# Kernel optimization log

Measured on AMD Instinct MI355X. Metric: run time of the kernel, lower is better.

The kernel has to match this reference:

```python
import jax, jax.numpy as jnp
import numpy as np
from jax import lax

XI = 2.0
RADIUS = int(3 * XI)  # 6 -> kernel size 13


def _gaussian_weight(xi: float):
    radius = int(3 * xi)
    coords = jnp.arange(-radius, radius + 1, dtype=jnp.float32)
    g1 = jnp.exp(-coords ** 2 / (2.0 * xi * xi))
    g1 = g1 / g1.sum()
    g3 = g1[:, None, None] * g1[None, :, None] * g1[None, None, :]  # (K,K,K)
    # grouped conv weight: (out_ch=3, in_ch/groups=1, K, K, K), same kernel per channel
    return jnp.broadcast_to(g3[None, None], (3, 1) + g3.shape)


def setup_inputs() -> dict:
    key = jax.random.key(0)
    x = jax.random.normal(key, (1, 3, 192, 192, 192), dtype=jnp.float32)
    w = _gaussian_weight(XI)
    return {"x": x, "w": w}


def reference(x, w):
    # depthwise (groups=3) 3D cross-correlation with 'same' padding = radius,
    # matching nn.Conv3d(3, 3, (K,K,K), padding=radius, groups=3, bias=False)
    r = (w.shape[-1] - 1) // 2
    return lax.conv_general_dilated(
        x, w,
        window_strides=(1, 1, 1),
        padding=[(r, r)] * 3,
        dimension_numbers=("NCDHW", "OIDHW", "NCDHW"),
        feature_group_count=3,
    )
```

## Files before the change

kernel.cpp:

```cpp
#include <hip/hip_runtime.h>

#define RAD 6
#define KS 13
#define DIM 192
#define CH 3
#define W4C 48
#define PLANE4 (DIM * W4C)
#define VOL4 (DIM * PLANE4)
#define VOL (DIM * DIM * DIM)
#define TOTAL (CH * VOL)

__global__ void g1_extract_kernel(const float* __restrict__ w, float* __restrict__ g1) {
    int i = threadIdx.x;
    if (i < KS) {
        float s = 0.f;
        for (int j = 0; j < KS * KS; ++j) s += w[i * KS * KS + j];
        g1[i] = s;
    }
}

#define HT 32
#define HL 48
#define NT1 192
#define NLD (HL * W4C)

__global__ __launch_bounds__(NT1) void conv_wh2(const float* __restrict__ in,
                                                float* __restrict__ out,
                                                const float* __restrict__ g1) {
    __shared__ float4 tile[NLD];
    const int bid = blockIdx.x;
    const int ht = bid % 6;
    const int d = (bid / 6) % DIM;
    const int c = bid / (6 * DIM);
    const int h0 = ht * HT;
    const int t = threadIdx.x;

    float g[KS];
#pragma unroll
    for (int k = 0; k < KS; ++k) g[k] = g1[k];

    const float4* in4 = (const float4*)in;
    float4* out4 = (float4*)out;
    const size_t plane = (size_t)c * VOL4 + (size_t)d * PLANE4;
    const float4 z4 = make_float4(0.f, 0.f, 0.f, 0.f);

#pragma unroll
    for (int i = 0; i < 12; ++i) {
        int idx = t + i * NT1;
        int row = idx / W4C, w4 = idx % W4C;
        int h = h0 - 8 + row;
        int hc = min(max(h, 0), DIM - 1);
        float4 v = in4[plane + (size_t)hc * W4C + w4];
        if (h < 0 || h >= DIM) v = z4;
        tile[idx] = v;
    }
    __syncthreads();

    float4 va[12];
#pragma unroll
    for (int i = 0; i < 12; ++i) {
        int idx = t + i * NT1;
        int row = idx / W4C, w4 = idx % W4C;
        int w0 = w4 * 4;
        float f[20];
#pragma unroll
        for (int b = 0; b < 5; ++b) {
            int j = min(max(w4 + b - 2, 0), W4C - 1);
            float4 v = tile[row * W4C + j];
            f[4 * b + 0] = v.x; f[4 * b + 1] = v.y;
            f[4 * b + 2] = v.z; f[4 * b + 3] = v.w;
        }
#pragma unroll
        for (int j = 0; j < 20; ++j) {
            int ww = w0 - 8 + j;
            if (ww < 0 || ww >= DIM) f[j] = 0.f;
        }
        float4 o = z4;
#pragma unroll
        for (int k = 0; k < KS; ++k) {
            o.x += g[k] * f[k + 2];
            o.y += g[k] * f[k + 3];
            o.z += g[k] * f[k + 4];
            o.w += g[k] * f[k + 5];
        }
        va[i] = o;
    }
    __syncthreads();
#pragma unroll
    for (int i = 0; i < 12; ++i) tile[t + i * NT1] = va[i];
    __syncthreads();

    const int w4 = t % W4C;
    const int rg = t / W4C;
    const int i0 = rg * 8;
    float4 buf[KS];
#pragma unroll
    for (int j = 0; j < KS; ++j) buf[j] = tile[(i0 + 2 + j) * W4C + w4];

#pragma unroll
    for (int ii = 0; ii < 8; ++ii) {
        float4 a = z4;
#pragma unroll
        for (int j = 0; j < KS; ++j) {
            const float4 v = buf[(ii + j) % KS];
            float gw = g[j];
            a.x += gw * v.x; a.y += gw * v.y; a.z += gw * v.z; a.w += gw * v.w;
        }
        out4[plane + (size_t)(h0 + i0 + ii) * W4C + w4] = a;
        if (ii < 7) buf[ii % KS] = tile[(i0 + ii + 15) * W4C + w4];
    }
}

__global__ __launch_bounds__(256) void conv_d8(const float* __restrict__ in,
                                               float* __restrict__ out,
                                               const float* __restrict__ g1) {
    __shared__ float4 tile[DIM * 8];
    const int bid = blockIdx.x;
    const int wt = bid % 6;
    const int h = (bid / 6) % DIM;
    const int c = bid / (6 * DIM);
    const int t = threadIdx.x;

    float g[KS];
#pragma unroll
    for (int k = 0; k < KS; ++k) g[k] = g1[k];

    const float4* in4 = (const float4*)in;
    float4* out4 = (float4*)out;
    const size_t base4 = (size_t)c * VOL4 + (size_t)h * W4C + wt * 8;
    const float4 z4 = make_float4(0.f, 0.f, 0.f, 0.f);

#pragma unroll
    for (int i = 0; i < 6; ++i) {
        int idx = t + i * 256;
        int dd = idx / 8, w = idx % 8;
        tile[idx] = in4[base4 + (size_t)dd * PLANE4 + w];
    }
    __syncthreads();

    const int w = t % 8;
    const int seg = t / 8;
    const int d0 = seg * 6;

    float4 buf[KS];
#pragma unroll
    for (int j = 0; j < KS; ++j) {
        int p = d0 - RAD + j;
        buf[j] = (p >= 0 && p < DIM) ? tile[p * 8 + w] : z4;
    }

#pragma unroll
    for (int i = 0; i < 6; ++i) {
        float4 a = z4;
#pragma unroll
        for (int j = 0; j < KS; ++j) {
            const float4 v = buf[(i + j) % KS];
            float gw = g[j];
            a.x += gw * v.x; a.y += gw * v.y; a.z += gw * v.z; a.w += gw * v.w;
        }
        out4[base4 + (size_t)(d0 + i) * PLANE4 + w] = a;
        if (i < 5) {
            int p = d0 + i + RAD + 1;
            buf[i % KS] = (p < DIM) ? tile[p * 8 + w] : z4;
        }
    }
}

__global__ void naive_conv3d_kernel(const float* __restrict__ x, const float* __restrict__ w,
                                    float* __restrict__ out, int total) {
    int n = blockIdx.x * blockDim.x + threadIdx.x;
    if (n >= total) return;
    int wp = n % DIM;
    int h = (n / DIM) % DIM;
    int d = (n / (DIM * DIM)) % DIM;
    int c = n / (DIM * DIM * DIM);
    const float* wc = w + c * KS * KS * KS;
    const float* xc = x + (size_t)c * DIM * DIM * DIM;
    float acc = 0.f;
    for (int kd = 0; kd < KS; ++kd) {
        int dd = d + kd - RAD;
        if (dd < 0 || dd >= DIM) continue;
        for (int kh = 0; kh < KS; ++kh) {
            int hh = h + kh - RAD;
            if (hh < 0 || hh >= DIM) continue;
            for (int kw = 0; kw < KS; ++kw) {
                int ww = wp + kw - RAD;
                if (ww < 0 || ww >= DIM) continue;
                acc += wc[(kd * KS + kh) * KS + kw] * xc[((size_t)dd * DIM + hh) * DIM + ww];
            }
        }
    }
    out[n] = acc;
}

extern "C" void kernel_launch(void* const* d_in, const int* in_sizes, int n_in,
                              void* d_out, int out_size, void* d_ws, size_t ws_size,
                              hipStream_t stream) {
    const float* x = (const float*)d_in[0];
    const float* w = (const float*)d_in[1];
    float* out = (float*)d_out;

    const size_t inter_bytes = (size_t)TOTAL * sizeof(float);

    if (ws_size >= inter_bytes + 64) {
        float* inter = (float*)d_ws;
        float* g1 = (float*)((char*)d_ws + inter_bytes);

        g1_extract_kernel<<<1, 64, 0, stream>>>(w, g1);

        conv_wh2<<<CH * DIM * 6, NT1, 0, stream>>>(x, inter, g1);

        conv_d8<<<CH * DIM * 6, 256, 0, stream>>>(inter, out, g1);
    } else {
        const int threads = 256;
        const int blocks = (TOTAL + threads - 1) / threads;
        naive_conv3d_kernel<<<blocks, threads, 0, stream>>>(x, w, out, TOTAL);
    }
}
```

Baseline: 191.0 us.

## Fold 1D weight extraction into conv kernels and read W-pass directly from global

```diff
diff --git a/kernel.cpp b/kernel.cpp
--- a/kernel.cpp
+++ b/kernel.cpp
@@ -10,34 +10,33 @@
 #define VOL (DIM * DIM * DIM)
 #define TOTAL (CH * VOL)
 
-__global__ void g1_extract_kernel(const float* __restrict__ w, float* __restrict__ g1) {
-    int i = threadIdx.x;
-    if (i < KS) {
-        float s = 0.f;
-        for (int j = 0; j < KS * KS; ++j) s += w[i * KS * KS + j];
-        g1[i] = s;
-    }
-}
-
-#define HT 32
-#define HL 48
+#define HT1 32
+#define HL1 44
 #define NT1 192
-#define NLD (HL * W4C)
-
-__global__ __launch_bounds__(NT1) void conv_wh2(const float* __restrict__ in,
+#define NLD1 (HL1 * W4C)
+
+__global__ __launch_bounds__(NT1) void conv_wh3(const float* __restrict__ in,
                                                 float* __restrict__ out,
-                                                const float* __restrict__ g1) {
-    __shared__ float4 tile[NLD];
+                                                const float* __restrict__ wk) {
+    __shared__ float4 tile[NLD1];
+    __shared__ float gS[KS];
     const int bid = blockIdx.x;
     const int ht = bid % 6;
     const int d = (bid / 6) % DIM;
     const int c = bid / (6 * DIM);
-    const int h0 = ht * HT;
+    const int h0 = ht * HT1;
     const int t = threadIdx.x;
 
+    if (t < KS) {
+        float s = 0.f;
+        for (int j = 0; j < KS * KS; ++j) s += wk[t * KS * KS + j];
+        gS[t] = s;
+    }
+    __syncthreads();
+
     float g[KS];
 #pragma unroll
-    for (int k = 0; k < KS; ++k) g[k] = g1[k];
+    for (int k = 0; k < KS; ++k) g[k] = gS[k];
 
     const float4* in4 = (const float4*)in;
     float4* out4 = (float4*)out;
@@ -45,31 +44,21 @@
     const float4 z4 = make_float4(0.f, 0.f, 0.f, 0.f);
 
 #pragma unroll
-    for (int i = 0; i < 12; ++i) {
+    for (int i = 0; i < 11; ++i) {
         int idx = t + i * NT1;
         int row = idx / W4C, w4 = idx % W4C;
-        int h = h0 - 8 + row;
+        int h = h0 - RAD + row;
         int hc = min(max(h, 0), DIM - 1);
-        float4 v = in4[plane + (size_t)hc * W4C + w4];
-        if (h < 0 || h >= DIM) v = z4;
-        tile[idx] = v;
-    }
-    __syncthreads();
-
-    float4 va[12];
-#pragma unroll
-    for (int i = 0; i < 12; ++i) {
-        int idx = t + i * NT1;
-        int row = idx / W4C, w4 = idx % W4C;
-        int w0 = w4 * 4;
+        const float4* rp = in4 + plane + (size_t)hc * W4C;
         float f[20];
 #pragma unroll
         for (int b = 0; b < 5; ++b) {
             int j = min(max(w4 + b - 2, 0), W4C - 1);
-            float4 v = tile[row * W4C + j];
+            float4 v = rp[j];
             f[4 * b + 0] = v.x; f[4 * b + 1] = v.y;
             f[4 * b + 2] = v.z; f[4 * b + 3] = v.w;
         }
+        int w0 = w4 * 4;
 #pragma unroll
         for (int j = 0; j < 20; ++j) {
             int ww = w0 - 8 + j;
@@ -83,11 +72,9 @@
             o.z += g[k] * f[k + 4];
             o.w += g[k] * f[k + 5];
         }
-        va[i] = o;
-    }
-    __syncthreads();
-#pragma unroll
-    for (int i = 0; i < 12; ++i) tile[t + i * NT1] = va[i];
+        if (h < 0 || h >= DIM) o = z4;
+        tile[idx] = o;
+    }
     __syncthreads();
 
     const int w4 = t % W4C;
@@ -95,7 +82,7 @@
     const int i0 = rg * 8;
     float4 buf[KS];
 #pragma unroll
-    for (int j = 0; j < KS; ++j) buf[j] = tile[(i0 + 2 + j) * W4C + w4];
+    for (int j = 0; j < KS; ++j) buf[j] = tile[(i0 + j) * W4C + w4];
 
 #pragma unroll
     for (int ii = 0; ii < 8; ++ii) {
@@ -107,23 +94,26 @@
             a.x += gw * v.x; a.y += gw * v.y; a.z += gw * v.z; a.w += gw * v.w;
         }
         out4[plane + (size_t)(h0 + i0 + ii) * W4C + w4] = a;
-        if (ii < 7) buf[ii % KS] = tile[(i0 + ii + 15) * W4C + w4];
+        if (ii < 7) buf[ii % KS] = tile[(i0 + ii + KS) * W4C + w4];
     }
 }
 
 __global__ __launch_bounds__(256) void conv_d8(const float* __restrict__ in,
                                                float* __restrict__ out,
-                                               const float* __restrict__ g1) {
+                                               const float* __restrict__ wk) {
     __shared__ float4 tile[DIM * 8];
+    __shared__ float gS[KS];
     const int bid = blockIdx.x;
     const int wt = bid % 6;
     const int h = (bid / 6) % DIM;
     const int c = bid / (6 * DIM);
     const int t = threadIdx.x;
 
-    float g[KS];
-#pragma unroll
-    for (int k = 0; k < KS; ++k) g[k] = g1[k];
+    if (t < KS) {
+        float s = 0.f;
+        for (int j = 0; j < KS * KS; ++j) s += wk[t * KS * KS + j];
+        gS[t] = s;
+    }
 
     const float4* in4 = (const float4*)in;
     float4* out4 = (float4*)out;
@@ -137,6 +127,10 @@
         tile[idx] = in4[base4 + (size_t)dd * PLANE4 + w];
     }
     __syncthreads();
+
+    float g[KS];
+#pragma unroll
+    for (int k = 0; k < KS; ++k) g[k] = gS[k];
 
     const int w = t % 8;
     const int seg = t / 8;
@@ -202,15 +196,12 @@
 
     const size_t inter_bytes = (size_t)TOTAL * sizeof(float);
 
-    if (ws_size >= inter_bytes + 64) {
+    if (ws_size >= inter_bytes) {
         float* inter = (float*)d_ws;
-        float* g1 = (float*)((char*)d_ws + inter_bytes);
-
-        g1_extract_kernel<<<1, 64, 0, stream>>>(w, g1);
-
-        conv_wh2<<<CH * DIM * 6, NT1, 0, stream>>>(x, inter, g1);
-
-        conv_d8<<<CH * DIM * 6, 256, 0, stream>>>(inter, out, g1);
+
+        conv_wh3<<<CH * DIM * 6, NT1, 0, stream>>>(x, inter, w);
+
+        conv_d8<<<CH * DIM * 6, 256, 0, stream>>>(inter, out, w);
     } else {
         const int threads = 256;
         const int blocks = (TOTAL + threads - 1) / threads;
```

After: 208.8 us. +9.3%, slower.
